# Kernel tuning notes

Hardware: AMD Instinct MI355X
Metric: run time of the kernel (lower is better)

The kernel has to match this reference:

```python
import jax, jax.numpy as jnp
import numpy as np

N_NODES = 50000
N_EDGES = 1_600_000
N_GRAPHS = 512
WIDTH = 64
LAYERS = 4
NUM_FEAT = 2
NUM_CLASSES = 2


def _glorot(key, shape):
    fan_in, fan_out = shape[0], shape[1]
    lim = jnp.sqrt(6.0 / (fan_in + fan_out))
    return jax.random.uniform(key, shape, jnp.float32, -lim, lim)


def setup_inputs() -> dict:
    key = jax.random.key(0)
    ks = jax.random.split(key, 16)
    x = jax.random.normal(ks[0], (N_NODES, NUM_FEAT), jnp.float32)
    edge_index = jax.random.randint(ks[1], (2, N_EDGES), 0, N_NODES, jnp.int64)
    # equal partition of nodes into graphs so every pooling segment is nonempty
    batch = (jnp.arange(N_NODES, dtype=jnp.int64) * N_GRAPHS) // N_NODES
    W1 = _glorot(ks[2], (NUM_FEAT, 32)); b1 = jnp.zeros((32,), jnp.float32)
    W2 = _glorot(ks[3], (32, WIDTH));    b2 = jnp.zeros((WIDTH,), jnp.float32)
    convW = jnp.stack([_glorot(ks[4 + i], (WIDTH, WIDTH)) for i in range(LAYERS)])
    convB = jnp.zeros((LAYERS, WIDTH), jnp.float32)
    fcW1 = _glorot(ks[9], (WIDTH, WIDTH));   fcb1 = jnp.zeros((WIDTH,), jnp.float32)
    fcW2 = _glorot(ks[10], (WIDTH, 32));     fcb2 = jnp.zeros((32,), jnp.float32)
    fcW3 = _glorot(ks[11], (32, NUM_CLASSES)); fcb3 = jnp.zeros((NUM_CLASSES,), jnp.float32)
    return dict(x=x, edge_index=edge_index, batch=batch,
                W1=W1, b1=b1, W2=W2, b2=b2, convW=convW, convB=convB,
                fcW1=fcW1, fcb1=fcb1, fcW2=fcW2, fcb2=fcb2, fcW3=fcW3, fcb3=fcb3)


def _gcn(x, W, b, src, dst, dinv):
    # GCNConv with added self-loops and symmetric normalization
    xw = x @ W  # [N, out]
    coef = dinv[src] * dinv[dst]  # [E]
    agg = jax.ops.segment_sum(xw[src] * coef[:, None], dst, num_segments=N_NODES)
    return agg + xw * (dinv * dinv)[:, None] + b


def reference(x, edge_index, batch, W1, b1, W2, b2, convW, convB,
              fcW1, fcb1, fcW2, fcb2, fcW3, fcb3):
    src, dst = edge_index[0], edge_index[1]
    # degree with self-loops (edge weight 1), computed on target nodes
    deg = jax.ops.segment_sum(jnp.ones_like(dst, dtype=x.dtype), dst,
                              num_segments=N_NODES) + 1.0
    dinv = jax.lax.rsqrt(deg)
    h = jax.nn.elu(_gcn(x, W1, b1, src, dst, dinv))   # [N, 32]
    h = jax.nn.elu(_gcn(h, W2, b2, src, dst, dinv))   # [N, WIDTH]
    for l in range(LAYERS):
        h = jax.nn.elu(_gcn(h, convW[l], convB[l], src, dst, dinv))
    # scatter_max pooling over graphs
    g = jax.ops.segment_max(h, batch, num_segments=N_GRAPHS)  # [G, WIDTH]
    g = jax.nn.elu(g @ fcW1 + fcb1)
    # dropout in eval mode is identity
    g = jax.nn.elu(g @ fcW2 + fcb2)
    g = g @ fcW3 + fcb3
    return jax.nn.log_softmax(g, axis=1)
```

## Files before the change

kernel.cpp:

```cpp
#include <hip/hip_runtime.h>
#include <hip/hip_bf16.h>


#define N_NODES 50000
#define N_GRAPHS 512
#define WIDTH 64
#define NBUCK 196
#define BINBLK 256

#define OFF_W1   0
#define OFF_B1   64
#define OFF_W2   96
#define OFF_B2   2144
#define OFF_CW   2208
#define OFF_CB   18592
#define OFF_FW1  18848
#define OFF_FB1  22944
#define OFF_FW2  23008
#define OFF_FB2  25056
#define OFF_FW3  25088
#define OFF_FB3  25152
#define TOTAL_W  25154
#define TOTAL_X  100000
#define TOTAL_CVT (TOTAL_X + TOTAL_W)

__device__ __forceinline__ float elu_f(float x) {
    return x > 0.f ? x : expm1f(x);
}

__device__ __forceinline__ unsigned fmono(float v) {
    unsigned b = __float_as_uint(v);
    return (b & 0x80000000u) ? ~b : (b | 0x80000000u);
}
__device__ __forceinline__ float funmono(unsigned m) {
    unsigned b = (m & 0x80000000u) ? (m ^ 0x80000000u) : ~m;
    return __uint_as_float(b);
}

__device__ __forceinline__ float blo(unsigned u) { return __uint_as_float(u << 16); }
__device__ __forceinline__ float bhi(unsigned u) { return __uint_as_float(u & 0xFFFF0000u); }

__global__ void detect_kernel(const void* __restrict__ eidx,
                              const void* __restrict__ x,
                              int* __restrict__ flags) {
    const int* e32 = (const int*)eidx;
    int i64 = ((e32[1] | e32[3] | e32[5] | e32[7]) == 0) ? 1 : 0;
    const unsigned short* h = (const unsigned short*)x;
    int cnt = 0;
    for (int i = 0; i < 32; ++i) {
        unsigned b = (h[2 * i] >> 8) & 0x7F;
        if (b >= 0x3C && b <= 0x42) cnt++;
    }
    flags[0] = i64;
    flags[1] = (cnt >= 16) ? 1 : 0;
}

struct CvtArgs {
    const void* src[13];
    int off[13];
    int total;
};

__global__ void cvt_all_kernel(CvtArgs a, float* __restrict__ out,
                               const int* __restrict__ flags) {
    const int bf = flags[1];
    for (int idx = blockIdx.x * blockDim.x + threadIdx.x; idx < a.total;
         idx += gridDim.x * blockDim.x) {
        int t = 0;
        for (int k = 1; k < 13; ++k) if (idx >= a.off[k]) t = k;
        int i = idx - a.off[t];
        float v = bf ? __bfloat162float(((const __hip_bfloat16*)a.src[t])[i])
                     : ((const float*)a.src[t])[i];
        out[idx] = v;
    }
}

__global__ void cvt_batch_kernel(const void* __restrict__ in, int* __restrict__ out,
                                 int n, const int* __restrict__ flags) {
    int i = blockIdx.x * blockDim.x + threadIdx.x;
    if (i >= n) return;
    out[i] = flags[0] ? (int)((const long long*)in)[i] : ((const int*)in)[i];
}

__device__ __forceinline__ int eidx_read(const void* eidx, long long i, int is64) {
    return is64 ? (int)((const long long*)eidx)[i] : ((const int*)eidx)[i];
}

__global__ __launch_bounds__(256) void histA_kernel(const void* __restrict__ eidx, int E,
                                                    int* __restrict__ gtable,
                                                    const int* __restrict__ flags) {
    __shared__ int hist[NBUCK];
    const int t = threadIdx.x, blk = blockIdx.x;
    if (t < NBUCK) hist[t] = 0;
    __syncthreads();
    const int chunk = (E + BINBLK - 1) / BINBLK;
    const int e0 = blk * chunk, e1 = min(E, e0 + chunk);
    const int is64 = flags[0];
    for (int e = e0 + t; e < e1; e += 256) {
        int d = eidx_read(eidx, (long long)E + e, is64);
        atomicAdd(&hist[d >> 8], 1);
    }
    __syncthreads();
    if (t < NBUCK) gtable[t * BINBLK + blk] = hist[t];
}

__global__ void scan_a_kernel(const int* __restrict__ in, int* __restrict__ out,
                              int* __restrict__ bsum, int n) {
    __shared__ int s[256];
    int i = blockIdx.x * 256 + threadIdx.x;
    int v = (i < n) ? in[i] : 0;
    s[threadIdx.x] = v;
    __syncthreads();
    for (int o = 1; o < 256; o <<= 1) {
        int t = (threadIdx.x >= o) ? s[threadIdx.x - o] : 0;
        __syncthreads();
        s[threadIdx.x] += t;
        __syncthreads();
    }
    if (i < n) out[i] = s[threadIdx.x] - v;
    if (threadIdx.x == 255) bsum[blockIdx.x] = s[255];
}

__global__ void scan_b_kernel(int* __restrict__ bsum, int NB) {
    __shared__ int s[256];
    int v = (threadIdx.x < NB) ? bsum[threadIdx.x] : 0;
    s[threadIdx.x] = v;
    __syncthreads();
    for (int o = 1; o < 256; o <<= 1) {
        int t = (threadIdx.x >= o) ? s[threadIdx.x - o] : 0;
        __syncthreads();
        s[threadIdx.x] += t;
        __syncthreads();
    }
    if (threadIdx.x < NB) bsum[threadIdx.x] = s[threadIdx.x] - v;
}

__global__ void scan_c_kernel(int* __restrict__ arr, const int* __restrict__ bsum, int n) {
    int i = blockIdx.x * 256 + threadIdx.x;
    if (i < n) arr[i] += bsum[i >> 8];
}

__global__ __launch_bounds__(256) void binC_kernel(const void* __restrict__ eidx, int E,
                                                   const int* __restrict__ gscan,
                                                   unsigned* __restrict__ binned,
                                                   const int* __restrict__ flags) {
    __shared__ int cur[NBUCK];
    const int t = threadIdx.x, blk = blockIdx.x;
    if (t < NBUCK) cur[t] = gscan[t * BINBLK + blk];
    __syncthreads();
    const int chunk = (E + BINBLK - 1) / BINBLK;
    const int e0 = blk * chunk, e1 = min(E, e0 + chunk);
    const int is64 = flags[0];
    for (int e = e0 + t; e < e1; e += 256) {
        int s = eidx_read(eidx, e, is64);
        int d = eidx_read(eidx, (long long)E + e, is64);
        int pos = atomicAdd(&cur[d >> 8], 1);
        binned[pos] = (unsigned)s | ((unsigned)d << 16);
    }
}

__global__ __launch_bounds__(256) void binD_kernel(const int* __restrict__ gscan,
                                                   const unsigned* __restrict__ binned,
                                                   int* __restrict__ rowPtr,
                                                   float* __restrict__ dinv,
                                                   unsigned short* __restrict__ csr_src,
                                                   int N, int E) {
    __shared__ int cnt[256];
    __shared__ int scn[256];
    __shared__ int cur[256];
    const int b = blockIdx.x, t = threadIdx.x;
    const int base = b << 8;
    const int start = gscan[b * BINBLK];
    const int end = (b == NBUCK - 1) ? E : gscan[(b + 1) * BINBLK];
    cnt[t] = 0;
    __syncthreads();
    for (int i = start + t; i < end; i += 256)
        atomicAdd(&cnt[(binned[i] >> 16) - base], 1);
    __syncthreads();
    int c = cnt[t];
    scn[t] = c;
    __syncthreads();
    for (int o = 1; o < 256; o <<= 1) {
        int v = (t >= o) ? scn[t - o] : 0;
        __syncthreads();
        scn[t] += v;
        __syncthreads();
    }
    int excl = start + scn[t] - c;
    int node = base + t;
    if (node < N) {
        rowPtr[node] = excl;
        dinv[node] = rsqrtf((float)c + 1.0f);
    }
    if (b == NBUCK - 1 && t == 0) rowPtr[N] = E;
    cur[t] = excl;
    __syncthreads();
    for (int i = start + t; i < end; i += 256) {
        unsigned p = binned[i];
        int pos = atomicAdd(&cur[(p >> 16) - base], 1);
        csr_src[pos] = (unsigned short)(p & 0xFFFFu);
    }
}

__global__ void scale_x_kernel(const float* __restrict__ xf,
                               const float* __restrict__ dinv,
                               float* __restrict__ hp0, int n2) {
    int i = blockIdx.x * blockDim.x + threadIdx.x;
    if (i < n2) hp0[i] = xf[i] * dinv[i >> 1];
}

__global__ __launch_bounds__(256) void fused2_kernel(
    const int* __restrict__ rowPtr, const unsigned short* __restrict__ csr_src,
    const float* __restrict__ hp0, const float* __restrict__ dinv,
    const float* __restrict__ W, const float* __restrict__ bias,
    __hip_bfloat16* __restrict__ hp_out, int N) {
    __shared__ float Ws[64];
    __shared__ float bs[32];
    const int t = threadIdx.x;
    if (t < 64) Ws[t] = W[t];
    if (t < 32) bs[t] = bias[t];
    __syncthreads();
    const int wave = t >> 6, lane = t & 63;
    const int node = blockIdx.x * 4 + wave;
    if (node >= N) return;
    const int r0 = rowPtr[node], r1 = rowPtr[node + 1];
    float g0 = 0.f, g1 = 0.f;
    for (int e = r0 + lane; e < r1; e += 64) {
        int s = csr_src[e];
        float2 v = *(const float2*)&hp0[2 * s];
        g0 += v.x; g1 += v.y;
    }
    for (int o = 32; o; o >>= 1) {
        g0 += __shfl_xor(g0, o, 64);
        g1 += __shfl_xor(g1, o, 64);
    }
    const float2 self = *(const float2*)&hp0[2 * node];
    const float di = dinv[node];
    g0 = (g0 + self.x) * di;
    g1 = (g1 + self.y) * di;
    if (lane < 32) {
        float o = g0 * Ws[lane] + g1 * Ws[32 + lane] + bs[lane];
        hp_out[(size_t)node * 32 + lane] = __float2bfloat16(elu_f(o) * di);
    }
}

__global__ __launch_bounds__(256) void fused32_kernel(
    const int* __restrict__ rowPtr, const unsigned short* __restrict__ csr_src,
    const __hip_bfloat16* __restrict__ hp_in, const float* __restrict__ dinv,
    const float* __restrict__ W, const float* __restrict__ bias,
    __hip_bfloat16* __restrict__ hp_out, int N) {
    __shared__ float Ws[32 * 64];
    __shared__ float bs[64];
    __shared__ float hs[4 * 32];
    const int t = threadIdx.x;
    for (int i = t; i < 32 * 64; i += 256) Ws[i] = W[i];
    if (t < 64) bs[t] = bias[t];
    __syncthreads();
    const int wave = t >> 6, lane = t & 63;
    const int node = blockIdx.x * 4 + wave;
    if (node >= N) return;
    const int q = lane >> 4, fl = lane & 15;
    const int fl2 = fl << 1;
    const int r0 = rowPtr[node], r1 = rowPtr[node + 1];
    float a0 = 0.f, b0 = 0.f, a1 = 0.f, b1 = 0.f;
    int e = r0 + q;
    for (; e + 28 < r1; e += 32) {
        unsigned u0 = *(const unsigned*)&hp_in[(size_t)csr_src[e]      * 32 + fl2];
        unsigned u1 = *(const unsigned*)&hp_in[(size_t)csr_src[e + 4]  * 32 + fl2];
        unsigned u2 = *(const unsigned*)&hp_in[(size_t)csr_src[e + 8]  * 32 + fl2];
        unsigned u3 = *(const unsigned*)&hp_in[(size_t)csr_src[e + 12] * 32 + fl2];
        unsigned u4 = *(const unsigned*)&hp_in[(size_t)csr_src[e + 16] * 32 + fl2];
        unsigned u5 = *(const unsigned*)&hp_in[(size_t)csr_src[e + 20] * 32 + fl2];
        unsigned u6 = *(const unsigned*)&hp_in[(size_t)csr_src[e + 24] * 32 + fl2];
        unsigned u7 = *(const unsigned*)&hp_in[(size_t)csr_src[e + 28] * 32 + fl2];
        a0 += blo(u0); b0 += bhi(u0);
        a1 += blo(u1); b1 += bhi(u1);
        a0 += blo(u2); b0 += bhi(u2);
        a1 += blo(u3); b1 += bhi(u3);
        a0 += blo(u4); b0 += bhi(u4);
        a1 += blo(u5); b1 += bhi(u5);
        a0 += blo(u6); b0 += bhi(u6);
        a1 += blo(u7); b1 += bhi(u7);
    }
    for (; e < r1; e += 4) {
        unsigned u = *(const unsigned*)&hp_in[(size_t)csr_src[e] * 32 + fl2];
        a0 += blo(u); b0 += bhi(u);
    }
    float a = a0 + a1, b = b0 + b1;
    a += __shfl_xor(a, 16, 64); b += __shfl_xor(b, 16, 64);
    a += __shfl_xor(a, 32, 64); b += __shfl_xor(b, 32, 64);
    const float di = dinv[node];
    if (q == 0) {
        unsigned su = *(const unsigned*)&hp_in[(size_t)node * 32 + fl2];
        float2 w;
        w.x = (a + blo(su)) * di;
        w.y = (b + bhi(su)) * di;
        *(float2*)&hs[wave * 32 + fl2] = w;
    }
    float o = 0.f;
#pragma unroll
    for (int k = 0; k < 32; ++k) o += hs[wave * 32 + k] * Ws[k * 64 + lane];
    o += bs[lane];
    hp_out[(size_t)node * 64 + lane] = __float2bfloat16(elu_f(o) * di);
}

template<int LAST>
__global__ __launch_bounds__(256) void fused64_kernel(
    const int* __restrict__ rowPtr, const unsigned short* __restrict__ csr_src,
    const __hip_bfloat16* __restrict__ hp_in, const float* __restrict__ dinv,
    const float* __restrict__ W, const float* __restrict__ bias,
    __hip_bfloat16* __restrict__ hp_out, unsigned* __restrict__ pooled,
    const int* __restrict__ batch, int N) {
    __shared__ float Ws[64 * 64];
    __shared__ float bs[64];
    __shared__ float hs[4 * 64];
    const int t = threadIdx.x;
    {
        const float4* W4 = (const float4*)W;
        float4* Ws4 = (float4*)Ws;
        for (int i = t; i < 1024; i += 256) Ws4[i] = W4[i];
    }
    if (t < 64) bs[t] = bias[t];
    __syncthreads();
    const int wave = t >> 6, lane = t & 63;
    const int node = blockIdx.x * 4 + wave;
    if (node >= N) return;
    const int half = lane >> 5, fl = lane & 31;
    const int fl2 = fl << 1;
    const int r0 = rowPtr[node], r1 = rowPtr[node + 1];
    float a0 = 0.f, b0 = 0.f, a1 = 0.f, b1 = 0.f, a2 = 0.f, b2 = 0.f, a3 = 0.f, b3 = 0.f;
    int e = r0 + half;
    for (; e + 14 < r1; e += 16) {
        unsigned u0 = *(const unsigned*)&hp_in[(size_t)csr_src[e]      * 64 + fl2];
        unsigned u1 = *(const unsigned*)&hp_in[(size_t)csr_src[e + 2]  * 64 + fl2];
        unsigned u2 = *(const unsigned*)&hp_in[(size_t)csr_src[e + 4]  * 64 + fl2];
        unsigned u3 = *(const unsigned*)&hp_in[(size_t)csr_src[e + 6]  * 64 + fl2];
        unsigned u4 = *(const unsigned*)&hp_in[(size_t)csr_src[e + 8]  * 64 + fl2];
        unsigned u5 = *(const unsigned*)&hp_in[(size_t)csr_src[e + 10] * 64 + fl2];
        unsigned u6 = *(const unsigned*)&hp_in[(size_t)csr_src[e + 12] * 64 + fl2];
        unsigned u7 = *(const unsigned*)&hp_in[(size_t)csr_src[e + 14] * 64 + fl2];
        a0 += blo(u0); b0 += bhi(u0);
        a1 += blo(u1); b1 += bhi(u1);
        a2 += blo(u2); b2 += bhi(u2);
        a3 += blo(u3); b3 += bhi(u3);
        a0 += blo(u4); b0 += bhi(u4);
        a1 += blo(u5); b1 += bhi(u5);
        a2 += blo(u6); b2 += bhi(u6);
        a3 += blo(u7); b3 += bhi(u7);
    }
    for (; e < r1; e += 2) {
        unsigned u = *(const unsigned*)&hp_in[(size_t)csr_src[e] * 64 + fl2];
        a0 += blo(u); b0 += bhi(u);
    }
    float a = (a0 + a1) + (a2 + a3);
    float b = (b0 + b1) + (b2 + b3);
    a += __shfl_xor(a, 32, 64);
    b += __shfl_xor(b, 32, 64);
    const float di = dinv[node];
    if (half == 0) {
        unsigned su = *(const unsigned*)&hp_in[(size_t)node * 64 + fl2];
        float2 w;
        w.x = (a + blo(su)) * di;
        w.y = (b + bhi(su)) * di;
        *(float2*)&hs[wave * 64 + fl2] = w;
    }
    float o = 0.f;
#pragma unroll
    for (int k = 0; k < 64; ++k) o += hs[wave * 64 + k] * Ws[k * 64 + lane];
    o += bs[lane];
    float v = elu_f(o);
    if (LAST) {
        atomicMax(&pooled[batch[node] * 64 + lane], fmono(v));
    } else {
        hp_out[(size_t)node * 64 + lane] = __float2bfloat16(v * di);
    }
}

__global__ void fc_kernel(const unsigned* __restrict__ pooled,
                          const float* __restrict__ Wall,
                          void* __restrict__ out,
                          const int* __restrict__ flags) {
    __shared__ float g[64], y1[64], y2[32], z[2];
    const int bid = blockIdx.x, t = threadIdx.x;
    g[t] = funmono(pooled[bid * 64 + t]);
    __syncthreads();
    {
        float acc = Wall[OFF_FB1 + t];
        for (int k = 0; k < 64; ++k) acc += g[k] * Wall[OFF_FW1 + k * 64 + t];
        y1[t] = elu_f(acc);
    }
    __syncthreads();
    if (t < 32) {
        float acc = Wall[OFF_FB2 + t];
        for (int k = 0; k < 64; ++k) acc += y1[k] * Wall[OFF_FW2 + k * 32 + t];
        y2[t] = elu_f(acc);
    }
    __syncthreads();
    if (t < 2) {
        float acc = Wall[OFF_FB3 + t];
        for (int k = 0; k < 32; ++k) acc += y2[k] * Wall[OFF_FW3 + k * 2 + t];
        z[t] = acc;
    }
    __syncthreads();
    if (t < 2) {
        float m = fmaxf(z[0], z[1]);
        float l = m + logf(expf(z[0] - m) + expf(z[1] - m));
        float r = z[t] - l;
        if (flags[1]) ((__hip_bfloat16*)out)[bid * 2 + t] = __float2bfloat16(r);
        else          ((float*)out)[bid * 2 + t] = r;
    }
}

extern "C" void kernel_launch(void* const* d_in, const int* in_sizes, int n_in,
                              void* d_out, int out_size, void* d_ws, size_t ws_size,
                              hipStream_t stream) {
    const int N = in_sizes[0] / 2;
    const int E = in_sizes[1] / 2;
    const int NT = NBUCK * BINBLK;

    const void* x    = d_in[0];
    const void* eidx = d_in[1];
    const void* batch = d_in[2];

    char* ws = (char*)d_ws;
    size_t off = 0;
    auto alloc = [&](size_t bytes) { char* p = ws + off; off += (bytes + 255) & ~(size_t)255; return p; };
    int*   flags   = (int*)  alloc(2 * sizeof(int));
    float* xcvt    = (float*)alloc(TOTAL_CVT * sizeof(float));
    int*   batch32 = (int*)  alloc(N_NODES * sizeof(int));
    float* dinv    = (float*)alloc(N_NODES * sizeof(float));
    int*   rowPtr  = (int*)  alloc((N_NODES + 1) * sizeof(int));
    int*   gtable  = (int*)  alloc(NT * sizeof(int));
    int*   gscan   = (int*)  alloc(NT * sizeof(int));
    int*   gbsum   = (int*)  alloc(256 * sizeof(int));
    unsigned* pooled = (unsigned*)alloc(N_GRAPHS * WIDTH * sizeof(unsigned));
    unsigned* binned = (unsigned*)alloc((size_t)E * sizeof(unsigned));
    unsigned short* csr16 = (unsigned short*)alloc((size_t)E * sizeof(unsigned short));
    float* hp0     = (float*)alloc((size_t)N_NODES * 2 * sizeof(float));
    __hip_bfloat16* hpA = (__hip_bfloat16*)alloc((size_t)N_NODES * 64 * sizeof(__hip_bfloat16));
    __hip_bfloat16* hpB = (__hip_bfloat16*)alloc((size_t)N_NODES * 64 * sizeof(__hip_bfloat16));

    float* xf   = xcvt;
    float* Wall = xcvt + TOTAL_X;

    detect_kernel<<<1, 1, 0, stream>>>(eidx, x, flags);

    CvtArgs ca;
    ca.src[0] = x;        ca.off[0] = 0;
    ca.src[1] = d_in[3];  ca.off[1] = TOTAL_X + OFF_W1;
    ca.src[2] = d_in[4];  ca.off[2] = TOTAL_X + OFF_B1;
    ca.src[3] = d_in[5];  ca.off[3] = TOTAL_X + OFF_W2;
    ca.src[4] = d_in[6];  ca.off[4] = TOTAL_X + OFF_B2;
    ca.src[5] = d_in[7];  ca.off[5] = TOTAL_X + OFF_CW;
    ca.src[6] = d_in[8];  ca.off[6] = TOTAL_X + OFF_CB;
    ca.src[7] = d_in[9];  ca.off[7] = TOTAL_X + OFF_FW1;
    ca.src[8] = d_in[10]; ca.off[8] = TOTAL_X + OFF_FB1;
    ca.src[9] = d_in[11]; ca.off[9] = TOTAL_X + OFF_FW2;
    ca.src[10] = d_in[12]; ca.off[10] = TOTAL_X + OFF_FB2;
    ca.src[11] = d_in[13]; ca.off[11] = TOTAL_X + OFF_FW3;
    ca.src[12] = d_in[14]; ca.off[12] = TOTAL_X + OFF_FB3;
    ca.total = TOTAL_CVT;
    cvt_all_kernel<<<(TOTAL_CVT + 255) / 256, 256, 0, stream>>>(ca, xcvt, flags);
    cvt_batch_kernel<<<(N + 255) / 256, 256, 0, stream>>>(batch, batch32, N, flags);

    hipMemsetAsync(pooled, 0, N_GRAPHS * WIDTH * sizeof(unsigned), stream);

    histA_kernel<<<BINBLK, 256, 0, stream>>>(eidx, E, gtable, flags);
    scan_a_kernel<<<(NT + 255) / 256, 256, 0, stream>>>(gtable, gscan, gbsum, NT);
    scan_b_kernel<<<1, 256, 0, stream>>>(gbsum, (NT + 255) / 256);
    scan_c_kernel<<<(NT + 255) / 256, 256, 0, stream>>>(gscan, gbsum, NT);
    binC_kernel<<<BINBLK, 256, 0, stream>>>(eidx, E, gscan, binned, flags);
    binD_kernel<<<NBUCK, 256, 0, stream>>>(gscan, binned, rowPtr, dinv, csr16, N, E);

    scale_x_kernel<<<(2 * N + 255) / 256, 256, 0, stream>>>(xf, dinv, hp0, 2 * N);

    const int FG = (N + 3) / 4;
    fused2_kernel<<<FG, 256, 0, stream>>>(rowPtr, csr16, hp0, dinv,
        Wall + OFF_W1, Wall + OFF_B1, hpA, N);
    fused32_kernel<<<FG, 256, 0, stream>>>(rowPtr, csr16, hpA, dinv,
        Wall + OFF_W2, Wall + OFF_B2, hpB, N);
    fused64_kernel<0><<<FG, 256, 0, stream>>>(rowPtr, csr16, hpB, dinv,
        Wall + OFF_CW + 0 * 4096, Wall + OFF_CB + 0 * 64, hpA, nullptr, nullptr, N);
    fused64_kernel<0><<<FG, 256, 0, stream>>>(rowPtr, csr16, hpA, dinv,
        Wall + OFF_CW + 1 * 4096, Wall + OFF_CB + 1 * 64, hpB, nullptr, nullptr, N);
    fused64_kernel<0><<<FG, 256, 0, stream>>>(rowPtr, csr16, hpB, dinv,
        Wall + OFF_CW + 2 * 4096, Wall + OFF_CB + 2 * 64, hpA, nullptr, nullptr, N);
    fused64_kernel<1><<<FG, 256, 0, stream>>>(rowPtr, csr16, hpA, dinv,
        Wall + OFF_CW + 3 * 4096, Wall + OFF_CB + 3 * 64, nullptr, pooled, batch32, N);

    fc_kernel<<<N_GRAPHS, 64, 0, stream>>>(pooled, Wall, d_out, flags);
}
```

Measured before the change: 417.2 us.

## Preload neighbor indices per wave with shuffles and pack weights as bf16 pairs

Each wave loads up to 64 CSR neighbor indices in one coalesced read, then hands them out with cross-lane shuffles. This replaces the repeated per-lane scalar index loads in the gather loops, and the deeper unroll raises memory-level parallelism. The layer weights are also stored in shared memory as packed bf16 pairs, which halves LDS footprint and weight reads in the small matvec. The cost is lower weight precision and extra shuffle instructions.

```diff
diff --git a/kernel.cpp b/kernel.cpp
--- a/kernel.cpp
+++ b/kernel.cpp
@@ -40,6 +40,12 @@
 __device__ __forceinline__ float blo(unsigned u) { return __uint_as_float(u << 16); }
 __device__ __forceinline__ float bhi(unsigned u) { return __uint_as_float(u & 0xFFFF0000u); }
 
+__device__ __forceinline__ unsigned packbf2(float lo, float hi) {
+    __hip_bfloat16 l = __float2bfloat16(lo);
+    __hip_bfloat16 h = __float2bfloat16(hi);
+    return (unsigned)*(unsigned short*)&l | ((unsigned)*(unsigned short*)&h << 16);
+}
+
 __global__ void detect_kernel(const void* __restrict__ eidx,
                               const void* __restrict__ x,
                               int* __restrict__ flags) {
@@ -249,11 +255,14 @@
     const __hip_bfloat16* __restrict__ hp_in, const float* __restrict__ dinv,
     const float* __restrict__ W, const float* __restrict__ bias,
     __hip_bfloat16* __restrict__ hp_out, int N) {
-    __shared__ float Ws[32 * 64];
+    __shared__ unsigned Ws2[16 * 64];
     __shared__ float bs[64];
     __shared__ float hs[4 * 32];
     const int t = threadIdx.x;
-    for (int i = t; i < 32 * 64; i += 256) Ws[i] = W[i];
+    for (int i = t; i < 16 * 64; i += 256) {
+        int k2 = i >> 6, c = i & 63;
+        Ws2[i] = packbf2(W[(2 * k2) * 64 + c], W[(2 * k2 + 1) * 64 + c]);
+    }
     if (t < 64) bs[t] = bias[t];
     __syncthreads();
     const int wave = t >> 6, lane = t & 63;
@@ -262,29 +271,43 @@
     const int q = lane >> 4, fl = lane & 15;
     const int fl2 = fl << 1;
     const int r0 = rowPtr[node], r1 = rowPtr[node + 1];
+    const int deg = r1 - r0;
+    int myIdx = 0;
+    if (lane < deg) myIdx = csr_src[r0 + lane];
+    const int nreg = deg < 64 ? deg : 64;
     float a0 = 0.f, b0 = 0.f, a1 = 0.f, b1 = 0.f;
-    int e = r0 + q;
-    for (; e + 28 < r1; e += 32) {
-        unsigned u0 = *(const unsigned*)&hp_in[(size_t)csr_src[e]      * 32 + fl2];
-        unsigned u1 = *(const unsigned*)&hp_in[(size_t)csr_src[e + 4]  * 32 + fl2];
-        unsigned u2 = *(const unsigned*)&hp_in[(size_t)csr_src[e + 8]  * 32 + fl2];
-        unsigned u3 = *(const unsigned*)&hp_in[(size_t)csr_src[e + 12] * 32 + fl2];
-        unsigned u4 = *(const unsigned*)&hp_in[(size_t)csr_src[e + 16] * 32 + fl2];
-        unsigned u5 = *(const unsigned*)&hp_in[(size_t)csr_src[e + 20] * 32 + fl2];
-        unsigned u6 = *(const unsigned*)&hp_in[(size_t)csr_src[e + 24] * 32 + fl2];
-        unsigned u7 = *(const unsigned*)&hp_in[(size_t)csr_src[e + 28] * 32 + fl2];
-        a0 += blo(u0); b0 += bhi(u0);
-        a1 += blo(u1); b1 += bhi(u1);
-        a0 += blo(u2); b0 += bhi(u2);
-        a1 += blo(u3); b1 += bhi(u3);
-        a0 += blo(u4); b0 += bhi(u4);
-        a1 += blo(u5); b1 += bhi(u5);
-        a0 += blo(u6); b0 += bhi(u6);
-        a1 += blo(u7); b1 += bhi(u7);
-    }
-    for (; e < r1; e += 4) {
-        unsigned u = *(const unsigned*)&hp_in[(size_t)csr_src[e] * 32 + fl2];
-        a0 += blo(u); b0 += bhi(u);
+    int base = 0;
+    for (; base + 31 < nreg; base += 32) {
+        unsigned u[8];
+#pragma unroll
+        for (int s = 0; s < 8; ++s) {
+            int idx = __shfl(myIdx, base + 4 * s + q, 64);
+            u[s] = *(const unsigned*)&hp_in[(size_t)idx * 32 + fl2];
+        }
+#pragma unroll
+        for (int s = 0; s < 8; ++s) {
+            if (s & 1) { a1 += blo(u[s]); b1 += bhi(u[s]); }
+            else       { a0 += blo(u[s]); b0 += bhi(u[s]); }
+        }
+    }
+    for (; base + 3 < nreg; base += 4) {
+        int idx = __shfl(myIdx, base + q, 64);
+        unsigned uu = *(const unsigned*)&hp_in[(size_t)idx * 32 + fl2];
+        a0 += blo(uu); b0 += bhi(uu);
+    }
+    {
+        int rem = nreg - base;
+        int sel = base + (q < rem ? q : 0);
+        int idx = __shfl(myIdx, sel, 64);
+        if (q < rem) {
+            unsigned uu = *(const unsigned*)&hp_in[(size_t)idx * 32 + fl2];
+            a0 += blo(uu); b0 += bhi(uu);
+        }
+    }
+    for (int ee = 64 + q; ee < deg; ee += 4) {
+        int idx = csr_src[r0 + ee];
+        unsigned uu = *(const unsigned*)&hp_in[(size_t)idx * 32 + fl2];
+        a0 += blo(uu); b0 += bhi(uu);
     }
     float a = a0 + a1, b = b0 + b1;
     a += __shfl_xor(a, 16, 64); b += __shfl_xor(b, 16, 64);
@@ -299,7 +322,11 @@
     }
     float o = 0.f;
 #pragma unroll
-    for (int k = 0; k < 32; ++k) o += hs[wave * 32 + k] * Ws[k * 64 + lane];
+    for (int k2 = 0; k2 < 16; ++k2) {
+        float2 h2 = *(const float2*)&hs[wave * 32 + (k2 << 1)];
+        unsigned wp = Ws2[k2 * 64 + lane];
+        o += h2.x * blo(wp) + h2.y * bhi(wp);
+    }
     o += bs[lane];
     hp_out[(size_t)node * 64 + lane] = __float2bfloat16(elu_f(o) * di);
 }
@@ -311,14 +338,13 @@
     const float* __restrict__ W, const float* __restrict__ bias,
     __hip_bfloat16* __restrict__ hp_out, unsigned* __restrict__ pooled,
     const int* __restrict__ batch, int N) {
-    __shared__ float Ws[64 * 64];
+    __shared__ unsigned Ws2[32 * 64];
     __shared__ float bs[64];
     __shared__ float hs[4 * 64];
     const int t = threadIdx.x;
-    {
-        const float4* W4 = (const float4*)W;
-        float4* Ws4 = (float4*)Ws;
-        for (int i = t; i < 1024; i += 256) Ws4[i] = W4[i];
+    for (int i = t; i < 32 * 64; i += 256) {
+        int k2 = i >> 6, c = i & 63;
+        Ws2[i] = packbf2(W[(2 * k2) * 64 + c], W[(2 * k2 + 1) * 64 + c]);
     }
     if (t < 64) bs[t] = bias[t];
     __syncthreads();
@@ -328,29 +354,46 @@
     const int half = lane >> 5, fl = lane & 31;
     const int fl2 = fl << 1;
     const int r0 = rowPtr[node], r1 = rowPtr[node + 1];
-    float a0 = 0.f, b0 = 0.f, a1 = 0.f, b1 = 0.f, a2 = 0.f, b2 = 0.f, a3 = 0.f, b3 = 0.f;
-    int e = r0 + half;
-    for (; e + 14 < r1; e += 16) {
-        unsigned u0 = *(const unsigned*)&hp_in[(size_t)csr_src[e]      * 64 + fl2];
-        unsigned u1 = *(const unsigned*)&hp_in[(size_t)csr_src[e + 2]  * 64 + fl2];
-        unsigned u2 = *(const unsigned*)&hp_in[(size_t)csr_src[e + 4]  * 64 + fl2];
-        unsigned u3 = *(const unsigned*)&hp_in[(size_t)csr_src[e + 6]  * 64 + fl2];
-        unsigned u4 = *(const unsigned*)&hp_in[(size_t)csr_src[e + 8]  * 64 + fl2];
-        unsigned u5 = *(const unsigned*)&hp_in[(size_t)csr_src[e + 10] * 64 + fl2];
-        unsigned u6 = *(const unsigned*)&hp_in[(size_t)csr_src[e + 12] * 64 + fl2];
-        unsigned u7 = *(const unsigned*)&hp_in[(size_t)csr_src[e + 14] * 64 + fl2];
-        a0 += blo(u0); b0 += bhi(u0);
-        a1 += blo(u1); b1 += bhi(u1);
-        a2 += blo(u2); b2 += bhi(u2);
-        a3 += blo(u3); b3 += bhi(u3);
-        a0 += blo(u4); b0 += bhi(u4);
-        a1 += blo(u5); b1 += bhi(u5);
-        a2 += blo(u6); b2 += bhi(u6);
-        a3 += blo(u7); b3 += bhi(u7);
-    }
-    for (; e < r1; e += 2) {
-        unsigned u = *(const unsigned*)&hp_in[(size_t)csr_src[e] * 64 + fl2];
-        a0 += blo(u); b0 += bhi(u);
+    const int deg = r1 - r0;
+    int myIdx = 0;
+    if (lane < deg) myIdx = csr_src[r0 + lane];
+    const int nreg = deg < 64 ? deg : 64;
+    float a0 = 0.f, b0 = 0.f, a1 = 0.f, b1 = 0.f;
+    float a2 = 0.f, b2 = 0.f, a3 = 0.f, b3 = 0.f;
+    int base = 0;
+    for (; base + 31 < nreg; base += 32) {
+        unsigned u[16];
+#pragma unroll
+        for (int s = 0; s < 16; ++s) {
+            int idx = __shfl(myIdx, base + 2 * s + half, 64);
+            u[s] = *(const unsigned*)&hp_in[(size_t)idx * 64 + fl2];
+        }
+#pragma unroll
+        for (int s = 0; s < 16; ++s) {
+            switch (s & 3) {
+                case 0: a0 += blo(u[s]); b0 += bhi(u[s]); break;
+                case 1: a1 += blo(u[s]); b1 += bhi(u[s]); break;
+                case 2: a2 += blo(u[s]); b2 += bhi(u[s]); break;
+                default: a3 += blo(u[s]); b3 += bhi(u[s]); break;
+            }
+        }
+    }
+    for (; base + 1 < nreg; base += 2) {
+        int idx = __shfl(myIdx, base + half, 64);
+        unsigned uu = *(const unsigned*)&hp_in[(size_t)idx * 64 + fl2];
+        a0 += blo(uu); b0 += bhi(uu);
+    }
+    {
+        int idxL = __shfl(myIdx, nreg > 0 ? nreg - 1 : 0, 64);
+        if (base < nreg && half == 0) {
+            unsigned uu = *(const unsigned*)&hp_in[(size_t)idxL * 64 + fl2];
+            a0 += blo(uu); b0 += bhi(uu);
+        }
+    }
+    for (int ee = 64 + half; ee < deg; ee += 2) {
+        int idx = csr_src[r0 + ee];
+        unsigned uu = *(const unsigned*)&hp_in[(size_t)idx * 64 + fl2];
+        a0 += blo(uu); b0 += bhi(uu);
     }
     float a = (a0 + a1) + (a2 + a3);
     float b = (b0 + b1) + (b2 + b3);
@@ -366,7 +409,11 @@
     }
     float o = 0.f;
 #pragma unroll
-    for (int k = 0; k < 64; ++k) o += hs[wave * 64 + k] * Ws[k * 64 + lane];
+    for (int k2 = 0; k2 < 32; ++k2) {
+        float2 h2 = *(const float2*)&hs[wave * 64 + (k2 << 1)];
+        unsigned wp = Ws2[k2 * 64 + lane];
+        o += h2.x * blo(wp) + h2.y * bhi(wp);
+    }
     o += bs[lane];
     float v = elu_f(o);
     if (LAST) {
```

After: 458.6 us. 9.9% more time.

## Split 64-wide feature gathers into two 32-column passes over separate arrays

Applied to the files above, without the earlier changes.

Node features are now stored as two separate 32-column bf16 arrays. Each 64-wide GCN layer becomes two launches: one gathers neighbor sums for the first half into a float buffer, and the second gathers the other half, combines both, and applies the matmul. The aim is a smaller gathered working set per pass (3.2 MB instead of 6.4 MB) so random neighbor reads hit cache better. In exchange it adds a kernel launch per layer, reads the CSR twice and makes a float round-trip through aggP.

```diff
diff --git a/kernel.cpp b/kernel.cpp
--- a/kernel.cpp
+++ b/kernel.cpp
@@ -248,7 +248,7 @@
     const int* __restrict__ rowPtr, const unsigned short* __restrict__ csr_src,
     const __hip_bfloat16* __restrict__ hp_in, const float* __restrict__ dinv,
     const float* __restrict__ W, const float* __restrict__ bias,
-    __hip_bfloat16* __restrict__ hp_out, int N) {
+    __hip_bfloat16* __restrict__ out0, __hip_bfloat16* __restrict__ out1, int N) {
     __shared__ float Ws[32 * 64];
     __shared__ float bs[64];
     __shared__ float hs[4 * 32];
@@ -301,16 +301,71 @@
 #pragma unroll
     for (int k = 0; k < 32; ++k) o += hs[wave * 32 + k] * Ws[k * 64 + lane];
     o += bs[lane];
-    hp_out[(size_t)node * 64 + lane] = __float2bfloat16(elu_f(o) * di);
+    float w = elu_f(o) * di;
+    if (lane < 32) out0[(size_t)node * 32 + lane] = __float2bfloat16(w);
+    else           out1[(size_t)node * 32 + (lane - 32)] = __float2bfloat16(w);
+}
+
+__global__ __launch_bounds__(256) void gatherA_kernel(
+    const int* __restrict__ rowPtr, const unsigned short* __restrict__ csr_src,
+    const __hip_bfloat16* __restrict__ hp_half,
+    const float* __restrict__ dinv,
+    float* __restrict__ aggP,
+    int N) {
+    const int t = threadIdx.x;
+    const int wave = t >> 6, lane = t & 63;
+    const int node = blockIdx.x * 4 + wave;
+    if (node >= N) return;
+    const int q = lane >> 4, fl = lane & 15;
+    const int fl2 = fl << 1;
+    const int r0 = rowPtr[node], r1 = rowPtr[node + 1];
+    float a0 = 0.f, b0 = 0.f, a1 = 0.f, b1 = 0.f;
+    int e = r0 + q;
+    for (; e + 28 < r1; e += 32) {
+        unsigned u0 = *(const unsigned*)&hp_half[(size_t)csr_src[e]      * 32 + fl2];
+        unsigned u1 = *(const unsigned*)&hp_half[(size_t)csr_src[e + 4]  * 32 + fl2];
+        unsigned u2 = *(const unsigned*)&hp_half[(size_t)csr_src[e + 8]  * 32 + fl2];
+        unsigned u3 = *(const unsigned*)&hp_half[(size_t)csr_src[e + 12] * 32 + fl2];
+        unsigned u4 = *(const unsigned*)&hp_half[(size_t)csr_src[e + 16] * 32 + fl2];
+        unsigned u5 = *(const unsigned*)&hp_half[(size_t)csr_src[e + 20] * 32 + fl2];
+        unsigned u6 = *(const unsigned*)&hp_half[(size_t)csr_src[e + 24] * 32 + fl2];
+        unsigned u7 = *(const unsigned*)&hp_half[(size_t)csr_src[e + 28] * 32 + fl2];
+        a0 += blo(u0); b0 += bhi(u0);
+        a1 += blo(u1); b1 += bhi(u1);
+        a0 += blo(u2); b0 += bhi(u2);
+        a1 += blo(u3); b1 += bhi(u3);
+        a0 += blo(u4); b0 += bhi(u4);
+        a1 += blo(u5); b1 += bhi(u5);
+        a0 += blo(u6); b0 += bhi(u6);
+        a1 += blo(u7); b1 += bhi(u7);
+    }
+    for (; e < r1; e += 4) {
+        unsigned u = *(const unsigned*)&hp_half[(size_t)csr_src[e] * 32 + fl2];
+        a0 += blo(u); b0 += bhi(u);
+    }
+    float a = a0 + a1, b = b0 + b1;
+    a += __shfl_xor(a, 16, 64); b += __shfl_xor(b, 16, 64);
+    a += __shfl_xor(a, 32, 64); b += __shfl_xor(b, 32, 64);
+    if (q == 0) {
+        const float di = dinv[node];
+        unsigned su = *(const unsigned*)&hp_half[(size_t)node * 32 + fl2];
+        float2 w;
+        w.x = (a + blo(su)) * di;
+        w.y = (b + bhi(su)) * di;
+        *(float2*)&aggP[(size_t)node * 32 + fl2] = w;
+    }
 }
 
 template<int LAST>
-__global__ __launch_bounds__(256) void fused64_kernel(
+__global__ __launch_bounds__(256) void combineB_kernel(
     const int* __restrict__ rowPtr, const unsigned short* __restrict__ csr_src,
-    const __hip_bfloat16* __restrict__ hp_in, const float* __restrict__ dinv,
-    const float* __restrict__ W, const float* __restrict__ bias,
-    __hip_bfloat16* __restrict__ hp_out, unsigned* __restrict__ pooled,
-    const int* __restrict__ batch, int N) {
+    const __hip_bfloat16* __restrict__ hp_half,
+    const float* __restrict__ aggP,
+    const float* __restrict__ dinv,
+    const float* __restrict__ W,
+    const float* __restrict__ bias,
+    __hip_bfloat16* __restrict__ out0, __hip_bfloat16* __restrict__ out1,
+    unsigned* __restrict__ pooled, const int* __restrict__ batch, int N) {
     __shared__ float Ws[64 * 64];
     __shared__ float bs[64];
     __shared__ float hs[4 * 64];
@@ -325,44 +380,45 @@
     const int wave = t >> 6, lane = t & 63;
     const int node = blockIdx.x * 4 + wave;
     if (node >= N) return;
-    const int half = lane >> 5, fl = lane & 31;
+    const int q = lane >> 4, fl = lane & 15;
     const int fl2 = fl << 1;
     const int r0 = rowPtr[node], r1 = rowPtr[node + 1];
-    float a0 = 0.f, b0 = 0.f, a1 = 0.f, b1 = 0.f, a2 = 0.f, b2 = 0.f, a3 = 0.f, b3 = 0.f;
-    int e = r0 + half;
-    for (; e + 14 < r1; e += 16) {
-        unsigned u0 = *(const unsigned*)&hp_in[(size_t)csr_src[e]      * 64 + fl2];
-        unsigned u1 = *(const unsigned*)&hp_in[(size_t)csr_src[e + 2]  * 64 + fl2];
-        unsigned u2 = *(const unsigned*)&hp_in[(size_t)csr_src[e + 4]  * 64 + fl2];
-        unsigned u3 = *(const unsigned*)&hp_in[(size_t)csr_src[e + 6]  * 64 + fl2];
-        unsigned u4 = *(const unsigned*)&hp_in[(size_t)csr_src[e + 8]  * 64 + fl2];
-        unsigned u5 = *(const unsigned*)&hp_in[(size_t)csr_src[e + 10] * 64 + fl2];
-        unsigned u6 = *(const unsigned*)&hp_in[(size_t)csr_src[e + 12] * 64 + fl2];
-        unsigned u7 = *(const unsigned*)&hp_in[(size_t)csr_src[e + 14] * 64 + fl2];
+    float a0 = 0.f, b0 = 0.f, a1 = 0.f, b1 = 0.f;
+    int e = r0 + q;
+    for (; e + 28 < r1; e += 32) {
+        unsigned u0 = *(const unsigned*)&hp_half[(size_t)csr_src[e]      * 32 + fl2];
+        unsigned u1 = *(const unsigned*)&hp_half[(size_t)csr_src[e + 4]  * 32 + fl2];
+        unsigned u2 = *(const unsigned*)&hp_half[(size_t)csr_src[e + 8]  * 32 + fl2];
+        unsigned u3 = *(const unsigned*)&hp_half[(size_t)csr_src[e + 12] * 32 + fl2];
+        unsigned u4 = *(const unsigned*)&hp_half[(size_t)csr_src[e + 16] * 32 + fl2];
+        unsigned u5 = *(const unsigned*)&hp_half[(size_t)csr_src[e + 20] * 32 + fl2];
+        unsigned u6 = *(const unsigned*)&hp_half[(size_t)csr_src[e + 24] * 32 + fl2];
+        unsigned u7 = *(const unsigned*)&hp_half[(size_t)csr_src[e + 28] * 32 + fl2];
         a0 += blo(u0); b0 += bhi(u0);
         a1 += blo(u1); b1 += bhi(u1);
-        a2 += blo(u2); b2 += bhi(u2);
-        a3 += blo(u3); b3 += bhi(u3);
+        a0 += blo(u2); b0 += bhi(u2);
+        a1 += blo(u3); b1 += bhi(u3);
         a0 += blo(u4); b0 += bhi(u4);
         a1 += blo(u5); b1 += bhi(u5);
-        a2 += blo(u6); b2 += bhi(u6);
-        a3 += blo(u7); b3 += bhi(u7);
-    }
-    for (; e < r1; e += 2) {
-        unsigned u = *(const unsigned*)&hp_in[(size_t)csr_src[e] * 64 + fl2];
+        a0 += blo(u6); b0 += bhi(u6);
+        a1 += blo(u7); b1 += bhi(u7);
+    }
+    for (; e < r1; e += 4) {
+        unsigned u = *(const unsigned*)&hp_half[(size_t)csr_src[e] * 32 + fl2];
         a0 += blo(u); b0 += bhi(u);
     }
-    float a = (a0 + a1) + (a2 + a3);
-    float b = (b0 + b1) + (b2 + b3);
-    a += __shfl_xor(a, 32, 64);
-    b += __shfl_xor(b, 32, 64);
+    float a = a0 + a1, b = b0 + b1;
+    a += __shfl_xor(a, 16, 64); b += __shfl_xor(b, 16, 64);
+    a += __shfl_xor(a, 32, 64); b += __shfl_xor(b, 32, 64);
     const float di = dinv[node];
-    if (half == 0) {
-        unsigned su = *(const unsigned*)&hp_in[(size_t)node * 64 + fl2];
+    if (q == 0) {
+        unsigned su = *(const unsigned*)&hp_half[(size_t)node * 32 + fl2];
         float2 w;
         w.x = (a + blo(su)) * di;
         w.y = (b + bhi(su)) * di;
-        *(float2*)&hs[wave * 64 + fl2] = w;
+        *(float2*)&hs[wave * 64 + 32 + fl2] = w;
+        float2 p0 = *(const float2*)&aggP[(size_t)node * 32 + fl2];
+        *(float2*)&hs[wave * 64 + fl2] = p0;
     }
     float o = 0.f;
 #pragma unroll
@@ -372,7 +428,9 @@
     if (LAST) {
         atomicMax(&pooled[batch[node] * 64 + lane], fmono(v));
     } else {
-        hp_out[(size_t)node * 64 + lane] = __float2bfloat16(v * di);
+        float w = v * di;
+        if (lane < 32) out0[(size_t)node * 32 + lane] = __float2bfloat16(w);
+        else           out1[(size_t)node * 32 + (lane - 32)] = __float2bfloat16(w);
     }
 }
 
@@ -437,8 +495,12 @@
     unsigned* binned = (unsigned*)alloc((size_t)E * sizeof(unsigned));
     unsigned short* csr16 = (unsigned short*)alloc((size_t)E * sizeof(unsigned short));
     float* hp0     = (float*)alloc((size_t)N_NODES * 2 * sizeof(float));
-    __hip_bfloat16* hpA = (__hip_bfloat16*)alloc((size_t)N_NODES * 64 * sizeof(__hip_bfloat16));
-    __hip_bfloat16* hpB = (__hip_bfloat16*)alloc((size_t)N_NODES * 64 * sizeof(__hip_bfloat16));
+    __hip_bfloat16* h32 = (__hip_bfloat16*)alloc((size_t)N_NODES * 32 * sizeof(__hip_bfloat16));
+    __hip_bfloat16* hX0 = (__hip_bfloat16*)alloc((size_t)N_NODES * 32 * sizeof(__hip_bfloat16));
+    __hip_bfloat16* hX1 = (__hip_bfloat16*)alloc((size_t)N_NODES * 32 * sizeof(__hip_bfloat16));
+    __hip_bfloat16* hY0 = (__hip_bfloat16*)alloc((size_t)N_NODES * 32 * sizeof(__hip_bfloat16));
+    __hip_bfloat16* hY1 = (__hip_bfloat16*)alloc((size_t)N_NODES * 32 * sizeof(__hip_bfloat16));
+    float* aggP    = (float*)alloc((size_t)N_NODES * 32 * sizeof(float));
 
     float* xf   = xcvt;
     float* Wall = xcvt + TOTAL_X;
@@ -476,17 +538,21 @@
 
     const int FG = (N + 3) / 4;
     fused2_kernel<<<FG, 256, 0, stream>>>(rowPtr, csr16, hp0, dinv,
-        Wall + OFF_W1, Wall + OFF_B1, hpA, N);
-    fused32_kernel<<<FG, 256, 0, stream>>>(rowPtr, csr16, hpA, dinv,
-        Wall + OFF_W2, Wall + OFF_B2, hpB, N);
-    fused64_kernel<0><<<FG, 256, 0, stream>>>(rowPtr, csr16, hpB, dinv,
-        Wall + OFF_CW + 0 * 4096, Wall + OFF_CB + 0 * 64, hpA, nullptr, nullptr, N);
-    fused64_kernel<0><<<FG, 256, 0, stream>>>(rowPtr, csr16, hpA, dinv,
-        Wall + OFF_CW + 1 * 4096, Wall + OFF_CB + 1 * 64, hpB, nullptr, nullptr, N);
-    fused64_kernel<0><<<FG, 256, 0, stream>>>(rowPtr, csr16, hpB, dinv,
-        Wall + OFF_CW + 2 * 4096, Wall + OFF_CB + 2 * 64, hpA, nullptr, nullptr, N);
-    fused64_kernel<1><<<FG, 256, 0, stream>>>(rowPtr, csr16, hpA, dinv,
-        Wall + OFF_CW + 3 * 4096, Wall + OFF_CB + 3 * 64, nullptr, pooled, batch32, N);
+        Wall + OFF_W1, Wall + OFF_B1, h32, N);
+    fused32_kernel<<<FG, 256, 0, stream>>>(rowPtr, csr16, h32, dinv,
+        Wall + OFF_W2, Wall + OFF_B2, hX0, hX1, N);
+    gatherA_kernel<<<FG, 256, 0, stream>>>(rowPtr, csr16, hX0, dinv, aggP, N);
+    combineB_kernel<0><<<FG, 256, 0, stream>>>(rowPtr, csr16, hX1, aggP, dinv,
+        Wall + OFF_CW + 0 * 4096, Wall + OFF_CB + 0 * 64, hY0, hY1, nullptr, nullptr, N);
+    gatherA_kernel<<<FG, 256, 0, stream>>>(rowPtr, csr16, hY0, dinv, aggP, N);
+    combineB_kernel<0><<<FG, 256, 0, stream>>>(rowPtr, csr16, hY1, aggP, dinv,
+        Wall + OFF_CW + 1 * 4096, Wall + OFF_CB + 1 * 64, hX0, hX1, nullptr, nullptr, N);
+    gatherA_kernel<<<FG, 256, 0, stream>>>(rowPtr, csr16, hX0, dinv, aggP, N);
+    combineB_kernel<0><<<FG, 256, 0, stream>>>(rowPtr, csr16, hX1, aggP, dinv,
+        Wall + OFF_CW + 2 * 4096, Wall + OFF_CB + 2 * 64, hY0, hY1, nullptr, nullptr, N);
+    gatherA_kernel<<<FG, 256, 0, stream>>>(rowPtr, csr16, hY0, dinv, aggP, N);
+    combineB_kernel<1><<<FG, 256, 0, stream>>>(rowPtr, csr16, hY1, aggP, dinv,
+        Wall + OFF_CW + 3 * 4096, Wall + OFF_CB + 3 * 64, nullptr, nullptr, pooled, batch32, N);
 
     fc_kernel<<<N_GRAPHS, 64, 0, stream>>>(pooled, Wall, d_out, flags);
 }
```

Result: slower. 507.6 us (+21.7%).
